# Kernel tuning notes

Measured on AMD Instinct MI355X. Metric: run time of the kernel, lower is better.

The kernel has to match this reference:

```python
import jax, jax.numpy as jnp
import numpy as np

NEG_INF = -1e30  # stand-in for -inf before softmax (stable under fp16/bf16 too)


def setup_inputs() -> dict:
    key = jax.random.key(0)
    ks = jax.random.split(key, 6)
    B, T, C = 8, 2048, 384
    H, Dh = 6, 64
    s = 0.02
    return {
        "x": jax.random.normal(ks[0], (B, T, C), dtype=jnp.float32),
        "Wq": jax.random.normal(ks[1], (H, C, Dh), dtype=jnp.float32) * s,
        "Wk": jax.random.normal(ks[2], (H, C, Dh), dtype=jnp.float32) * s,
        "Wv": jax.random.normal(ks[3], (H, C, Dh), dtype=jnp.float32) * s,
        "Wp": jax.random.normal(ks[4], (C, C), dtype=jnp.float32) * s,
        "bp": jnp.zeros((C,), dtype=jnp.float32),
    }


def reference(x, Wq, Wk, Wv, Wp, bp):
    # x: [B, T, C]; Wq/Wk/Wv: [H, C, Dh] (per-head independent projections,
    # matching the torch ModuleList of Heads); Wp: [C, C]; bp: [C].
    B, T, C = x.shape
    H, _, Dh = Wq.shape
    scale = Dh ** -0.5  # torch uses self.head_size ** -0.5

    q = jnp.einsum('btc,hcd->bhtd', x, Wq)
    k = jnp.einsum('btc,hcd->bhtd', x, Wk)
    v = jnp.einsum('btc,hcd->bhtd', x, Wv)

    scores = jnp.einsum('bhtd,bhsd->bhts', q, k) * scale  # [B,H,T,T]
    causal = jnp.tril(jnp.ones((T, T), dtype=bool))       # tril mask
    scores = jnp.where(causal, scores, NEG_INF)
    wei = jax.nn.softmax(scores, axis=-1)
    # dropout layers are identity in eval mode

    out = jnp.einsum('bhts,bhsd->bhtd', wei, v)            # [B,H,T,Dh]
    out = out.transpose(0, 2, 1, 3).reshape(B, T, H * Dh)  # concat heads on last dim
    return out @ Wp + bp
```

## Files before the change

kernel.cpp:

```cpp
#include <hip/hip_runtime.h>
#include <hip/hip_bf16.h>

constexpr int T_ = 2048;
constexpr int C_ = 384;
constexpr int H_ = 6;
constexpr int D_ = 64;

typedef unsigned int u32;
typedef unsigned short u16;
typedef __attribute__((ext_vector_type(4))) float f32x4;
typedef __attribute__((ext_vector_type(16))) float f32x16;
typedef __attribute__((ext_vector_type(8))) short bf16x8;
typedef __attribute__((ext_vector_type(4))) short bf16x4;

__device__ __forceinline__ u32 f2bf(float f) {
  u32 u = __float_as_uint(f);
  return (u + 0x7FFFu + ((u >> 16) & 1u)) >> 16;
}
__device__ __forceinline__ u32 pk2(float a, float b) {
  return f2bf(a) | (f2bf(b) << 16);
}
__device__ __forceinline__ u32 pkcvt(float a, float b) {
  __hip_bfloat162 h = __float22bfloat162_rn(float2{a, b});
  return *(u32*)&h;
}
__device__ __forceinline__ void gload16(const u16* g, u16* l) {
  __builtin_amdgcn_global_load_lds(
      (const __attribute__((address_space(1))) u32*)g,
      (__attribute__((address_space(3))) u32*)l, 16, 0, 0);
}

constexpr float SC_ = 0.18033688011112042f;

__global__ __launch_bounds__(256) void xcvt_kernel(
    const float* __restrict__ x, u16* __restrict__ xb) {
  const int id = blockIdx.x * 256 + threadIdx.x;
  const float* s = x + (size_t)id * 8;
  f32x4 a = *(const f32x4*)s, b = *(const f32x4*)(s + 4);
  uint4 o;
  o.x = pkcvt(a[0], a[1]); o.y = pkcvt(a[2], a[3]);
  o.z = pkcvt(b[0], b[1]); o.w = pkcvt(b[2], b[3]);
  *(uint4*)(xb + (size_t)id * 8) = o;
}

__global__ __launch_bounds__(256) void convert_kernel(
    const float* __restrict__ Wq, const float* __restrict__ Wk,
    const float* __restrict__ Wv, const float* __restrict__ Wp,
    u16* __restrict__ Wt, u16* __restrict__ Wpt) {
  int id = blockIdx.x * 256 + threadIdx.x;
  if (id < 110592) {
    int n = id / 96, c0 = (id % 96) * 4;
    int mat = n / 384, nn = n % 384, h = nn >> 6, d = nn & 63;
    const float* W = (mat == 0) ? Wq : ((mat == 1) ? Wk : Wv);
    const float* s = W + (size_t)(h * C_ + c0) * D_ + d;
    uint2 o; o.x = pk2(s[0], s[64]); o.y = pk2(s[128], s[192]);
    *(uint2*)&Wt[(size_t)n * 384 + c0] = o;
  } else {
    int id2 = id - 110592;
    int n = id2 / 96, c0 = (id2 % 96) * 4;
    const float* s = Wp + (size_t)c0 * C_ + n;
    uint2 o; o.x = pk2(s[0], s[384]); o.y = pk2(s[768], s[1152]);
    *(uint2*)&Wpt[(size_t)n * 384 + c0] = o;
  }
}

#define GEMM_BODY(A_PTR, B_PTR)                                                \
  __shared__ u16 As[128 * 64], Bs[128 * 64];                                   \
  const int tid = threadIdx.x;                                                 \
  const int l = tid & 63, w = tid >> 6;                                        \
  const int wr = w >> 1, wc = w & 1;                                           \
  const int ql = l & 15, g = l >> 4;                                           \
  const int rc = l >> 3;                     \
  const int sgr = l & 7;                 \
  f32x4 acc[4][4];                                                             \
  _Pragma("unroll") for (int fi = 0; fi < 4; ++fi)                             \
  _Pragma("unroll") for (int fj = 0; fj < 4; ++fj) acc[fi][fj] = (f32x4)0.f;   \
  for (int kc = 0; kc < 6; ++kc) {                                             \
    if (kc) __syncthreads();                                                   \
    _Pragma("unroll") for (int c = 0; c < 4; ++c) {                            \
      const int rbase = w * 32 + c * 8;                                        \
      const int row = rbase + rc;                                              \
      const int gcol = (sgr ^ (row & 7)) * 8;     \
      gload16((A_PTR) + (size_t)(m0 + row) * 384 + kc * 64 + gcol,             \
              &As[rbase * 64]);                                                \
      gload16((B_PTR) + (size_t)(n0 + row) * 384 + kc * 64 + gcol,             \
              &Bs[rbase * 64]);                                                \
    }                                                                          \
    __syncthreads();                 \
    __builtin_amdgcn_s_setprio(1);                                             \
    _Pragma("unroll") for (int ks = 0; ks < 2; ++ks) {                         \
      bf16x8 af[4], bfr[4];                                                    \
      const int gl = ks * 4 + g;                                               \
      const int slot8 = (gl ^ (ql & 7)) * 8;                                   \
      _Pragma("unroll") for (int fi = 0; fi < 4; ++fi)                         \
        af[fi] = *(const bf16x8*)&As[(wr * 64 + fi * 16 + ql) * 64 + slot8];   \
      _Pragma("unroll") for (int fj = 0; fj < 4; ++fj)                         \
        bfr[fj] = *(const bf16x8*)&Bs[(wc * 64 + fj * 16 + ql) * 64 + slot8];  \
      _Pragma("unroll") for (int fi = 0; fi < 4; ++fi)                         \
      _Pragma("unroll") for (int fj = 0; fj < 4; ++fj)                         \
        acc[fi][fj] = __builtin_amdgcn_mfma_f32_16x16x32_bf16(                 \
            af[fi], bfr[fj], acc[fi][fj], 0, 0, 0);                            \
    }                                                                          \
    __builtin_amdgcn_s_setprio(0);                                             \
  }

__global__ __launch_bounds__(256) void gemm_qkv(
    const u16* __restrict__ xb, const u16* __restrict__ Wt,
    u16* __restrict__ Qb, u16* __restrict__ Kb, u16* __restrict__ Vtb) {
  const int bx = blockIdx.x;
  const int mt = bx / 9, nt = bx % 9;
  const int m0 = mt * 128, n0 = nt * 128;

  GEMM_BODY(xb, Wt)

  const int mat = nt / 3;
#pragma unroll
  for (int fi = 0; fi < 4; ++fi) {
    const int m = m0 + wr * 64 + fi * 16 + g * 4;
    const int b = m >> 11, t = m & 2047;
#pragma unroll
    for (int fj = 0; fj < 4; ++fj) {
      const int n = n0 + wc * 64 + fj * 16 + ql;
      const int nn = n - mat * 384, h = nn >> 6, d = nn & 63;
      if (mat == 0) {
        u16* dst = Qb + ((size_t)(b * H_ + h) * T_ + t) * D_ + d;
#pragma unroll
        for (int r = 0; r < 4; ++r)
          dst[(size_t)r * D_] = (u16)f2bf(acc[fi][fj][r] * SC_);
      } else if (mat == 1) {
        u16* dst = Kb + ((size_t)(b * H_ + h) * T_ + t) * D_ + d;
#pragma unroll
        for (int r = 0; r < 4; ++r) dst[(size_t)r * D_] = (u16)f2bf(acc[fi][fj][r]);
      } else {
        u16* dst = Vtb + ((size_t)(b * H_ + h) * D_ + d) * T_ + t;
        uint2 o;
        o.x = pkcvt(acc[fi][fj][0], acc[fi][fj][1]);
        o.y = pkcvt(acc[fi][fj][2], acc[fi][fj][3]);
        *(uint2*)dst = o;
      }
    }
  }
}

__global__ __launch_bounds__(256) void gemm_proj(
    const u16* __restrict__ attnb, const u16* __restrict__ Wpt,
    const float* __restrict__ bp, float* __restrict__ out) {
  const int bx = blockIdx.x;
  const int mt = bx / 3, nt = bx % 3;
  const int m0 = mt * 128, n0 = nt * 128;

  GEMM_BODY(attnb, Wpt)

#pragma unroll
  for (int fj = 0; fj < 4; ++fj) {
    const int n = n0 + wc * 64 + fj * 16 + ql;
    const float bias = bp[n];
#pragma unroll
    for (int fi = 0; fi < 4; ++fi) {
      const int m = m0 + wr * 64 + fi * 16 + g * 4;
#pragma unroll
      for (int r = 0; r < 4; ++r)
        out[(size_t)(m + r) * C_ + n] = acc[fi][fj][r] + bias;
    }
  }
}

__global__ __launch_bounds__(256) void attn_mfma_kernel(
    const u16* __restrict__ Qb, const u16* __restrict__ Kb,
    const u16* __restrict__ Vtb, u16* __restrict__ attnb) {
  __shared__ u16 Ks[2][64 * 64];
  __shared__ u16 Vs[2][64 * 64];
  const int tid = threadIdx.x;
  const int bx = blockIdx.x;
  const int qb = 15 - (bx / 48);
  const int bh = bx % 48;
  const int h = bh % H_, b = bh / H_;
  const int Q0 = qb * 128;
  const int nt = 2 * qb + 2;
  const size_t hb = (size_t)bh * T_ * D_;

  const int l = tid & 63, w = tid >> 6;
  const int hi = l >> 5, l31 = l & 31;
  const int qw0 = Q0 + w * 32;
  const int qrow = qw0 + l31;
  const int qwmax = qw0 + 31;
  const int rc = l >> 3;
  const int sgr = l & 7;

  bf16x8 qf[4];
  {
    const u16* qg = Qb + hb + (size_t)qrow * D_ + hi * 8;
#pragma unroll
    for (int cs = 0; cs < 4; ++cs) qf[cs] = *(const bf16x8*)(qg + cs * 16);
  }

#pragma unroll
  for (int c = 0; c < 2; ++c) {
    const int rbase = w * 16 + c * 8;
    const int row = rbase + rc;
    const int gc = (sgr ^ (row & 7)) * 8;
    gload16(Kb + hb + (size_t)row * D_ + gc, &Ks[0][rbase * 64]);
    gload16(Vtb + hb + (size_t)row * T_ + gc, &Vs[0][rbase * 64]);
  }
  __syncthreads();

  f32x16 oacc[2];
  oacc[0] = (f32x16)0.f; oacc[1] = (f32x16)0.f;
  float lrun = 0.f;
  const int swzA = (l31 & 7) * 8;

  for (int jt = 0; jt < nt; ++jt) {
    const int cur = jt & 1;
    if (jt + 1 < nt) {
      const int nb = cur ^ 1;
#pragma unroll
      for (int c = 0; c < 2; ++c) {
        const int rbase = w * 16 + c * 8;
        const int row = rbase + rc;
        const int gc = (sgr ^ (row & 7)) * 8;
        gload16(Kb + hb + (size_t)((jt + 1) * 64 + row) * D_ + gc,
                &Ks[nb][rbase * 64]);
        gload16(Vtb + hb + (size_t)row * T_ + (jt + 1) * 64 + gc,
                &Vs[nb][rbase * 64]);
      }
    }

    if (jt * 64 <= qwmax) {
      f32x16 sacc[2];
      sacc[0] = (f32x16)0.f; sacc[1] = (f32x16)0.f;
      __builtin_amdgcn_s_setprio(1);
#pragma unroll
      for (int kc = 0; kc < 2; ++kc)
#pragma unroll
        for (int cs = 0; cs < 4; ++cs) {
          bf16x8 kf = *(const bf16x8*)
              &Ks[cur][(kc * 32 + l31) * 64 + ((cs * 16 + 8 * hi) ^ swzA)];
          sacc[kc] = __builtin_amdgcn_mfma_f32_32x32x16_bf16(kf, qf[cs], sacc[kc], 0, 0, 0);
        }
      __builtin_amdgcn_s_setprio(0);

      float ps[32];
      if ((jt + 1) * 64 > qw0) {
#pragma unroll
        for (int kc = 0; kc < 2; ++kc)
#pragma unroll
          for (int r = 0; r < 16; ++r) {
            const int kglob = jt * 64 + kc * 32 + (r & 3) + 8 * (r >> 2) + 4 * hi;
            ps[kc * 16 + r] = __builtin_amdgcn_exp2f(
                kglob > qrow ? -1e30f : sacc[kc][r]);
          }
      } else {
#pragma unroll
        for (int kc = 0; kc < 2; ++kc)
#pragma unroll
          for (int r = 0; r < 16; ++r)
            ps[kc * 16 + r] = __builtin_amdgcn_exp2f(sacc[kc][r]);
      }

      float sm[16];
#pragma unroll
      for (int i = 0; i < 16; ++i) sm[i] = ps[i] + ps[i + 16];
#pragma unroll
      for (int i = 0; i < 8; ++i) sm[i] = sm[i] + sm[i + 8];
#pragma unroll
      for (int i = 0; i < 4; ++i) sm[i] = sm[i] + sm[i + 4];
      float rs = (sm[0] + sm[1]) + (sm[2] + sm[3]);
      rs += __shfl_xor(rs, 32);
      lrun += rs;

      u32 pw[4][4];
#pragma unroll
      for (int ks = 0; ks < 4; ++ks)
#pragma unroll
        for (int wd = 0; wd < 4; ++wd)
          pw[ks][wd] = pkcvt(ps[(ks >> 1) * 16 + (ks & 1) * 8 + 2 * wd],
                             ps[(ks >> 1) * 16 + (ks & 1) * 8 + 2 * wd + 1]);

      __builtin_amdgcn_s_setprio(1);
#pragma unroll
      for (int dc = 0; dc < 2; ++dc) {
#pragma unroll
        for (int ks = 0; ks < 4; ++ks) {
          const int rb = (dc * 32 + l31) * 64;
          bf16x4 v0 = *(const bf16x4*)&Vs[cur][rb + ((ks * 16 + 4 * hi) ^ swzA)];
          bf16x4 v1 = *(const bf16x4*)&Vs[cur][rb + ((ks * 16 + 4 * hi + 8) ^ swzA)];
          bf16x8 vf;
          *(bf16x4*)&vf = v0; *((bf16x4*)&vf + 1) = v1;
          bf16x8 pf;
          *(uint4*)&pf = make_uint4(pw[ks][0], pw[ks][1], pw[ks][2], pw[ks][3]);
          oacc[dc] = __builtin_amdgcn_mfma_f32_32x32x16_bf16(vf, pf, oacc[dc], 0, 0, 0);
        }
      }
      __builtin_amdgcn_s_setprio(0);
    }

    __syncthreads();
  }

  const float inv = 1.0f / lrun;
  u16* obase = attnb + ((size_t)(b * T_ + qrow)) * C_ + h * 64;
#pragma unroll
  for (int dc = 0; dc < 2; ++dc)
#pragma unroll
    for (int g4 = 0; g4 < 4; ++g4) {
      uint2 o;
      o.x = pkcvt(oacc[dc][g4 * 4 + 0] * inv, oacc[dc][g4 * 4 + 1] * inv);
      o.y = pkcvt(oacc[dc][g4 * 4 + 2] * inv, oacc[dc][g4 * 4 + 3] * inv);
      *(uint2*)(obase + dc * 32 + 8 * g4 + 4 * hi) = o;
    }
}

extern "C" void kernel_launch(void* const* d_in, const int* in_sizes, int n_in,
                              void* d_out, int out_size, void* d_ws, size_t ws_size,
                              hipStream_t stream) {
  (void)in_sizes; (void)n_in; (void)out_size; (void)ws_size;
  const float* x  = (const float*)d_in[0];
  const float* Wq = (const float*)d_in[1];
  const float* Wk = (const float*)d_in[2];
  const float* Wv = (const float*)d_in[3];
  const float* Wp = (const float*)d_in[4];
  const float* bp = (const float*)d_in[5];
  float* out = (float*)d_out;

  u16* Wt    = (u16*)d_ws;
  u16* Wpt   = Wt + 442368;
  u16* Qb    = Wpt + 147456;
  u16* Kb    = Qb + 6291456;
  u16* Vtb   = Kb + 6291456;
  u16* R     = Vtb + 6291456;
  u16* xb    = R;
  u16* attnb = R;

  xcvt_kernel<<<3072, 256, 0, stream>>>(x, xb);
  convert_kernel<<<576, 256, 0, stream>>>(Wq, Wk, Wv, Wp, Wt, Wpt);
  gemm_qkv<<<1152, 256, 0, stream>>>(xb, Wt, Qb, Kb, Vtb);
  attn_mfma_kernel<<<768, 256, 0, stream>>>(Qb, Kb, Vtb, attnb);
  gemm_proj<<<384, 256, 0, stream>>>(attnb, Wpt, bp, out);
}
```

Before: 112.4 us.

## Split long causal query tiles across two blocks with atomic-flag merge

Query tiles 8-15 in the causal attention kernel are split into two KV-range halves, each handled by its own block. A static schedule table interleaves these halves with the unsplit short tiles so the 1152 blocks are more evenly sized. Each half writes its unnormalized partial output in bf16 plus its row sum, and whichever block finishes second (found through an atomic counter) merges the two and normalizes. This targets the tail imbalance of the longest tiles, at the cost of extra partial-output traffic, a memset launch, and bf16 rounding of the partials before the merge.

```diff
diff --git a/kernel.cpp b/kernel.cpp
--- a/kernel.cpp
+++ b/kernel.cpp
@@ -20,6 +20,11 @@
 __device__ __forceinline__ u32 pk2(float a, float b) {
   return f2bf(a) | (f2bf(b) << 16);
 }
+__device__ __forceinline__ float bflo(u32 u) { return __uint_as_float(u << 16); }
+__device__ __forceinline__ float bfhi(u32 u) { return __uint_as_float(u & 0xFFFF0000u); }
+__device__ __forceinline__ float bfr(float v) {
+  return __uint_as_float(f2bf(v) << 16);
+}
 __device__ __forceinline__ u32 pkcvt(float a, float b) {
   __hip_bfloat162 h = __float22bfloat162_rn(float2{a, b});
   return *(u32*)&h;
@@ -31,6 +36,10 @@
 }
 
 constexpr float SC_ = 0.18033688011112042f;
+
+__device__ const int JQB[24] = {15,15, 7,14,14,13,13, 6,12,12,11,11, 5,10,10, 9, 9, 4, 8, 8, 3, 2, 1, 0};
+__device__ const int JK0[24] = { 0,16, 0, 0,15, 0,14, 0, 0,13, 0,12, 0, 0,11, 0,10, 0, 0, 9, 0, 0, 0, 0};
+__device__ const int JKN[24] = {16,32,16,15,30,14,28,14,13,26,12,24,12,11,22,10,20,10, 9,18, 8, 6, 4, 2};
 
 __global__ __launch_bounds__(256) void xcvt_kernel(
     const float* __restrict__ x, u16* __restrict__ xb) {
@@ -89,17 +98,17 @@
     __syncthreads();                 \
     __builtin_amdgcn_s_setprio(1);                                             \
     _Pragma("unroll") for (int ks = 0; ks < 2; ++ks) {                         \
-      bf16x8 af[4], bfr[4];                                                    \
+      bf16x8 af[4], bfr_[4];                                                   \
       const int gl = ks * 4 + g;                                               \
       const int slot8 = (gl ^ (ql & 7)) * 8;                                   \
       _Pragma("unroll") for (int fi = 0; fi < 4; ++fi)                         \
         af[fi] = *(const bf16x8*)&As[(wr * 64 + fi * 16 + ql) * 64 + slot8];   \
       _Pragma("unroll") for (int fj = 0; fj < 4; ++fj)                         \
-        bfr[fj] = *(const bf16x8*)&Bs[(wc * 64 + fj * 16 + ql) * 64 + slot8];  \
+        bfr_[fj] = *(const bf16x8*)&Bs[(wc * 64 + fj * 16 + ql) * 64 + slot8]; \
       _Pragma("unroll") for (int fi = 0; fi < 4; ++fi)                         \
       _Pragma("unroll") for (int fj = 0; fj < 4; ++fj)                         \
         acc[fi][fj] = __builtin_amdgcn_mfma_f32_16x16x32_bf16(                 \
-            af[fi], bfr[fj], acc[fi][fj], 0, 0, 0);                            \
+            af[fi], bfr_[fj], acc[fi][fj], 0, 0, 0);                           \
     }                                                                          \
     __builtin_amdgcn_s_setprio(0);                                             \
   }
@@ -167,16 +176,20 @@
 
 __global__ __launch_bounds__(256) void attn_mfma_kernel(
     const u16* __restrict__ Qb, const u16* __restrict__ Kb,
-    const u16* __restrict__ Vtb, u16* __restrict__ attnb) {
+    const u16* __restrict__ Vtb, u16* __restrict__ attnb,
+    u16* __restrict__ Opart, float* __restrict__ lpart,
+    int* __restrict__ flags) {
   __shared__ u16 Ks[2][64 * 64];
   __shared__ u16 Vs[2][64 * 64];
   const int tid = threadIdx.x;
   const int bx = blockIdx.x;
-  const int qb = 15 - (bx / 48);
+  const int rank = bx / 48;
   const int bh = bx % 48;
+  const int qb = JQB[rank];
+  const int jk0 = JK0[rank], jkn = JKN[rank];
+  const bool is_split = (qb >= 8);
   const int h = bh % H_, b = bh / H_;
   const int Q0 = qb * 128;
-  const int nt = 2 * qb + 2;
   const size_t hb = (size_t)bh * T_ * D_;
 
   const int l = tid & 63, w = tid >> 6;
@@ -199,8 +212,8 @@
     const int rbase = w * 16 + c * 8;
     const int row = rbase + rc;
     const int gc = (sgr ^ (row & 7)) * 8;
-    gload16(Kb + hb + (size_t)row * D_ + gc, &Ks[0][rbase * 64]);
-    gload16(Vtb + hb + (size_t)row * T_ + gc, &Vs[0][rbase * 64]);
+    gload16(Kb + hb + (size_t)(jk0 * 64 + row) * D_ + gc, &Ks[0][rbase * 64]);
+    gload16(Vtb + hb + (size_t)row * T_ + jk0 * 64 + gc, &Vs[0][rbase * 64]);
   }
   __syncthreads();
 
@@ -209,9 +222,10 @@
   float lrun = 0.f;
   const int swzA = (l31 & 7) * 8;
 
-  for (int jt = 0; jt < nt; ++jt) {
-    const int cur = jt & 1;
-    if (jt + 1 < nt) {
+  for (int jt = jk0; jt < jkn; ++jt) {
+    const int jj = jt - jk0;
+    const int cur = jj & 1;
+    if (jt + 1 < jkn) {
       const int nb = cur ^ 1;
 #pragma unroll
       for (int c = 0; c < 2; ++c) {
@@ -297,17 +311,61 @@
     __syncthreads();
   }
 
-  const float inv = 1.0f / lrun;
   u16* obase = attnb + ((size_t)(b * T_ + qrow)) * C_ + h * 64;
-#pragma unroll
-  for (int dc = 0; dc < 2; ++dc)
-#pragma unroll
-    for (int g4 = 0; g4 < 4; ++g4) {
-      uint2 o;
-      o.x = pkcvt(oacc[dc][g4 * 4 + 0] * inv, oacc[dc][g4 * 4 + 1] * inv);
-      o.y = pkcvt(oacc[dc][g4 * 4 + 2] * inv, oacc[dc][g4 * 4 + 3] * inv);
-      *(uint2*)(obase + dc * 32 + 8 * g4 + 4 * hi) = o;
+
+  if (!is_split) {
+    const float inv = 1.0f / lrun;
+#pragma unroll
+    for (int dc = 0; dc < 2; ++dc)
+#pragma unroll
+      for (int g4 = 0; g4 < 4; ++g4) {
+        uint2 o;
+        o.x = pkcvt(oacc[dc][g4 * 4 + 0] * inv, oacc[dc][g4 * 4 + 1] * inv);
+        o.y = pkcvt(oacc[dc][g4 * 4 + 2] * inv, oacc[dc][g4 * 4 + 3] * inv);
+        *(uint2*)(obase + dc * 32 + 8 * g4 + 4 * hi) = o;
+      }
+  } else {
+    const int qt = bh * 8 + (qb - 8);
+    const int halfid = (jk0 > 0) ? 1 : 0;
+    const int qloc = w * 32 + l31;
+    u16* mypart = halfid ? (Opart + ((size_t)qt * 128 + qloc) * 64) : obase;
+#pragma unroll
+    for (int dc = 0; dc < 2; ++dc)
+#pragma unroll
+      for (int g4 = 0; g4 < 4; ++g4) {
+        uint2 o;
+        o.x = pkcvt(oacc[dc][g4 * 4 + 0], oacc[dc][g4 * 4 + 1]);
+        o.y = pkcvt(oacc[dc][g4 * 4 + 2], oacc[dc][g4 * 4 + 3]);
+        *(uint2*)(mypart + dc * 32 + 8 * g4 + 4 * hi) = o;
+      }
+    if (hi == 0) lpart[(qt * 2 + halfid) * 128 + qloc] = lrun;
+    __threadfence();
+    __syncthreads();
+    __shared__ int dec;
+    if (tid == 0) dec = atomicAdd(&flags[qt], 1);
+    __syncthreads();
+    if (dec == 1) {
+      __threadfence();
+      const u16* otherO =
+          halfid ? obase : (Opart + ((size_t)qt * 128 + qloc) * 64);
+      const float lo = lpart[(qt * 2 + (halfid ^ 1)) * 128 + qloc];
+      const float inv = 1.0f / (lrun + lo);
+#pragma unroll
+      for (int dc = 0; dc < 2; ++dc)
+#pragma unroll
+        for (int g4 = 0; g4 < 4; ++g4) {
+          uint2 ov = *(const uint2*)(otherO + dc * 32 + 8 * g4 + 4 * hi);
+          const float s0 = bfr(oacc[dc][g4 * 4 + 0]) + bflo(ov.x);
+          const float s1 = bfr(oacc[dc][g4 * 4 + 1]) + bfhi(ov.x);
+          const float s2 = bfr(oacc[dc][g4 * 4 + 2]) + bflo(ov.y);
+          const float s3 = bfr(oacc[dc][g4 * 4 + 3]) + bfhi(ov.y);
+          uint2 o;
+          o.x = pkcvt(s0 * inv, s1 * inv);
+          o.y = pkcvt(s2 * inv, s3 * inv);
+          *(uint2*)(obase + dc * 32 + 8 * g4 + 4 * hi) = o;
+        }
     }
+  }
 }
 
 extern "C" void kernel_launch(void* const* d_in, const int* in_sizes, int n_in,
@@ -330,10 +388,14 @@
   u16* R     = Vtb + 6291456;
   u16* xb    = R;
   u16* attnb = R;
-
+  u16* Opart = R + 6291456;
+  float* lpart = (float*)(Opart + 3145728);
+  int* flags = (int*)(lpart + 98304);
+
+  hipMemsetAsync(flags, 0, 384 * sizeof(int), stream);
   xcvt_kernel<<<3072, 256, 0, stream>>>(x, xb);
   convert_kernel<<<576, 256, 0, stream>>>(Wq, Wk, Wv, Wp, Wt, Wpt);
   gemm_qkv<<<1152, 256, 0, stream>>>(xb, Wt, Qb, Kb, Vtb);
-  attn_mfma_kernel<<<768, 256, 0, stream>>>(Qb, Kb, Vtb, attnb);
+  attn_mfma_kernel<<<1152, 256, 0, stream>>>(Qb, Kb, Vtb, attnb, Opart, lpart, flags);
   gemm_proj<<<384, 256, 0, stream>>>(attnb, Wpt, bp, out);
 }
```

After: 284.9 us. 153% more time.

## Double attention query tile to 256 rows with 512-thread blocks sharing K/V tiles

Applied to the files above, without the earlier changes.

The attention kernel now uses 8 waves per block covering 256 query rows instead of 4 waves covering 128, halving the grid to 384 blocks. Each K/V tile staged in shared memory is reused by twice as many query rows, and each thread issues one staging load per tile instead of two. The cost is coarser causal work balance: fewer, larger blocks with more uneven per-block work, and lower-row waves sitting idle through the block-wide syncs of tiles they skip. The GEMM macro variable rename is cosmetic.

```diff
diff --git a/kernel.cpp b/kernel.cpp
--- a/kernel.cpp
+++ b/kernel.cpp
@@ -89,17 +89,17 @@
     __syncthreads();                 \
     __builtin_amdgcn_s_setprio(1);                                             \
     _Pragma("unroll") for (int ks = 0; ks < 2; ++ks) {                         \
-      bf16x8 af[4], bfr[4];                                                    \
+      bf16x8 af[4], bfr_[4];                                                   \
       const int gl = ks * 4 + g;                                               \
       const int slot8 = (gl ^ (ql & 7)) * 8;                                   \
       _Pragma("unroll") for (int fi = 0; fi < 4; ++fi)                         \
         af[fi] = *(const bf16x8*)&As[(wr * 64 + fi * 16 + ql) * 64 + slot8];   \
       _Pragma("unroll") for (int fj = 0; fj < 4; ++fj)                         \
-        bfr[fj] = *(const bf16x8*)&Bs[(wc * 64 + fj * 16 + ql) * 64 + slot8];  \
+        bfr_[fj] = *(const bf16x8*)&Bs[(wc * 64 + fj * 16 + ql) * 64 + slot8]; \
       _Pragma("unroll") for (int fi = 0; fi < 4; ++fi)                         \
       _Pragma("unroll") for (int fj = 0; fj < 4; ++fj)                         \
         acc[fi][fj] = __builtin_amdgcn_mfma_f32_16x16x32_bf16(                 \
-            af[fi], bfr[fj], acc[fi][fj], 0, 0, 0);                            \
+            af[fi], bfr_[fj], acc[fi][fj], 0, 0, 0);                           \
     }                                                                          \
     __builtin_amdgcn_s_setprio(0);                                             \
   }
@@ -165,18 +165,18 @@
   }
 }
 
-__global__ __launch_bounds__(256) void attn_mfma_kernel(
+__global__ __launch_bounds__(512) void attn_mfma_kernel(
     const u16* __restrict__ Qb, const u16* __restrict__ Kb,
     const u16* __restrict__ Vtb, u16* __restrict__ attnb) {
   __shared__ u16 Ks[2][64 * 64];
   __shared__ u16 Vs[2][64 * 64];
   const int tid = threadIdx.x;
   const int bx = blockIdx.x;
-  const int qb = 15 - (bx / 48);
+  const int qb = 7 - (bx / 48);
   const int bh = bx % 48;
   const int h = bh % H_, b = bh / H_;
-  const int Q0 = qb * 128;
-  const int nt = 2 * qb + 2;
+  const int Q0 = qb * 256;
+  const int nt = 4 * qb + 4;
   const size_t hb = (size_t)bh * T_ * D_;
 
   const int l = tid & 63, w = tid >> 6;
@@ -186,6 +186,8 @@
   const int qwmax = qw0 + 31;
   const int rc = l >> 3;
   const int sgr = l & 7;
+  const int srow = w * 8 + rc;
+  const int sgc = (sgr ^ (srow & 7)) * 8;
 
   bf16x8 qf[4];
   {
@@ -194,14 +196,8 @@
     for (int cs = 0; cs < 4; ++cs) qf[cs] = *(const bf16x8*)(qg + cs * 16);
   }
 
-#pragma unroll
-  for (int c = 0; c < 2; ++c) {
-    const int rbase = w * 16 + c * 8;
-    const int row = rbase + rc;
-    const int gc = (sgr ^ (row & 7)) * 8;
-    gload16(Kb + hb + (size_t)row * D_ + gc, &Ks[0][rbase * 64]);
-    gload16(Vtb + hb + (size_t)row * T_ + gc, &Vs[0][rbase * 64]);
-  }
+  gload16(Kb + hb + (size_t)srow * D_ + sgc, &Ks[0][(w * 8) * 64]);
+  gload16(Vtb + hb + (size_t)srow * T_ + sgc, &Vs[0][(w * 8) * 64]);
   __syncthreads();
 
   f32x16 oacc[2];
@@ -213,16 +209,10 @@
     const int cur = jt & 1;
     if (jt + 1 < nt) {
       const int nb = cur ^ 1;
-#pragma unroll
-      for (int c = 0; c < 2; ++c) {
-        const int rbase = w * 16 + c * 8;
-        const int row = rbase + rc;
-        const int gc = (sgr ^ (row & 7)) * 8;
-        gload16(Kb + hb + (size_t)((jt + 1) * 64 + row) * D_ + gc,
-                &Ks[nb][rbase * 64]);
-        gload16(Vtb + hb + (size_t)row * T_ + (jt + 1) * 64 + gc,
-                &Vs[nb][rbase * 64]);
-      }
+      gload16(Kb + hb + (size_t)((jt + 1) * 64 + srow) * D_ + sgc,
+              &Ks[nb][(w * 8) * 64]);
+      gload16(Vtb + hb + (size_t)srow * T_ + (jt + 1) * 64 + sgc,
+              &Vs[nb][(w * 8) * 64]);
     }
 
     if (jt * 64 <= qwmax) {
@@ -334,6 +324,6 @@
   xcvt_kernel<<<3072, 256, 0, stream>>>(x, xb);
   convert_kernel<<<576, 256, 0, stream>>>(Wq, Wk, Wv, Wp, Wt, Wpt);
   gemm_qkv<<<1152, 256, 0, stream>>>(xb, Wt, Qb, Kb, Vtb);
-  attn_mfma_kernel<<<768, 256, 0, stream>>>(Qb, Kb, Vtb, attnb);
+  attn_mfma_kernel<<<384, 512, 0, stream>>>(Qb, Kb, Vtb, attnb);
   gemm_proj<<<384, 256, 0, stream>>>(attnb, Wpt, bp, out);
 }
```

Measured after the change: 118.5 us. 1.05x slower.
